# Kernel optimization log

Measured on AMD Instinct MI355X. Metric: run time of the kernel, lower is better.

The kernel has to match this reference:

```python
import jax, jax.numpy as jnp
import numpy as np

B, L, C = 8, 256, 64
NEG = -1e30  # large negative instead of -inf to keep grads NaN-free


def setup_inputs() -> dict:
    key = jax.random.key(0)
    k1, k2 = jax.random.split(key)
    scores = jax.random.normal(k1, (B, L, L, C), dtype=jnp.float32)
    lens = jax.random.randint(k2, (B,), 64, L, dtype=jnp.int32)  # sentence lengths in [64, L-1]
    return {"scores": scores, "lens": lens}


def _inside_max(scores, lens):
    """Max-semiring CKY inside pass. scores: [B,L,L,C]; returns logZ per batch [B]."""
    t = jnp.transpose(jnp.max(scores, axis=-1), (1, 2, 0))  # [L,L,B] best label per span
    s0 = jnp.zeros((L, L, B), scores.dtype)                 # chart s[i,j] = best score of span (i,j)
    i = jnp.arange(L)
    j = jnp.arange(L)

    def step(s, w):
        e = jnp.clip(i + w, 0, L - 1)                       # span end, [L]
        k = jnp.clip(i[:, None] + j[None, :], 0, L - 1)     # split points, [L,L]
        left = s[i[:, None], k]                             # s[i, i+j], [L,L,B]
        right = s[k, e[:, None]]                            # s[i+j, i+w], [L,L,B]
        valid = (j[None, :] >= 1) & (j[None, :] < w) & ((i + w) < L)[:, None]
        comb = jnp.max(jnp.where(valid[..., None], left + right, NEG), axis=1)  # [L,B]
        s_l = t[i, e]                                       # label-max span score, [L,B]
        diag = jnp.where(w == 1, s_l, comb + s_l)
        row_ok = ((i + w) < L)[:, None]
        upd = jnp.where(row_ok, diag, s[i, e])
        s = s.at[i, e].set(upd)
        return s, None

    s, _ = jax.lax.scan(step, s0, jnp.arange(1, L))
    lens_c = jnp.clip(lens, 1, L - 1)
    return s[0, lens_c, jnp.arange(B)]                      # logZ (best tree score) per sentence


def reference(scores, lens):
    return _inside_max(scores, lens)
```

## Files before the change

kernel.cpp:

```cpp
#include <hip/hip_runtime.h>

#define LVAL 256
#define T    32
#define ST   36
#define SLAB (T * ST)
#define NB   8
#define NEG  (-1e30f)

#define LDS_FENCE() asm volatile("s_waitcnt lgkmcnt(0)" ::: "memory")

__device__ __forceinline__ size_t sidx(int b, int i, int e) {
    return ((size_t)b << 16) + (i << 8) + e;
}

template<int CTRL>
__device__ __forceinline__ float dpp_max(float v) {
#if __has_builtin(__builtin_amdgcn_mov_dpp)
    int o = __builtin_amdgcn_mov_dpp(__builtin_bit_cast(int, v), CTRL, 0xF, 0xF, true);
    return fmaxf(v, __builtin_bit_cast(float, o));
#else
    return fmaxf(v, __shfl_xor(v, CTRL == 0xB1 ? 1 : 2));
#endif
}

__global__ __launch_bounds__(256) void phase1(const float* __restrict__ scores,
                                              float* __restrict__ s,
                                              int* __restrict__ bar) {
    if (blockIdx.x == 0 && blockIdx.y == 0) {
        for (int k = threadIdx.x; k < 2048; k += 256) bar[k] = 0;
    }
    const int i = blockIdx.x, b = blockIdx.y;
    const int sub = threadIdx.x & 15, slot = threadIdx.x >> 4;
    const float* row = scores + ((((size_t)b * LVAL + i) * LVAL) << 6);
    #pragma unroll 4
    for (int m0 = 0; m0 < LVAL; m0 += 16) {
        const int e = m0 + slot;
        if (e > i) {
            float4 v = *((const float4*)(row + ((size_t)e << 6)) + sub);
            float mx = fmaxf(fmaxf(v.x, v.y), fmaxf(v.z, v.w));
            #pragma unroll
            for (int d = 1; d < 16; d <<= 1) mx = fmaxf(mx, __shfl_xor(mx, d));
            if (sub == 0) s[sidx(b, i, e)] = mx;
        }
    }
}

template<int LP>
__device__ __forceinline__ void diag_step(int lane, int l,
                                          float (*cur)[ST], float (*curT)[ST],
                                          const float (*tb)[ST]) {
    const int cells = T - l;
    const int P = 1 << LP;
    const int c = lane >> LP, p = lane & (P - 1);
    const bool guard = c < cells;
    const int li = guard ? c : 0;
    const int le = guard ? c + l : 0;
    constexpr int NF = 8 >> LP;
    const float tv = tb[li][le];
    float acc = NEG;
    #pragma unroll
    for (int m = 0; m < NF; ++m) {
        const int k0 = 4 * (p + m * P);
        float4 cu = *(const float4*)&cur[li][k0];
        float4 ct = *(const float4*)&curT[le][k0];
        acc = fmaxf(acc, fmaxf(fmaxf(cu.x + ct.x, cu.y + ct.y),
                               fmaxf(cu.z + ct.z, cu.w + ct.w)));
    }
    acc = dpp_max<0xB1>(acc);
    if (LP >= 2) acc = dpp_max<0x4E>(acc);
    const float v = acc + tv;
    if (guard && p == 0) cur[li][le] = v;
    if (guard && p == 1) curT[le][li] = v;
}

template<int LP>
__device__ __forceinline__ void edge_step(int lane, int l, int D,
                                          const float (*Ae)[ST], const float (*BeT)[ST],
                                          float (*cur)[ST], float (*curT)[ST],
                                          const float (*tb)[ST], const float (*pre)[ST]) {
    const int delta = l - (T - 1);
    const int ad = delta < 0 ? -delta : delta;
    const int cells = T - ad;
    const int P = 1 << LP;
    const int c = lane >> LP, p = lane & (P - 1);
    const bool guard = c < cells;
    const int li = guard ? (delta < 0 ? c + ad : c) : 0;
    const int le = guard ? li + delta : 0;
    constexpr int NF = 8 >> LP;
    const float tv = tb[li][le];
    float acc = pre[li][le];
    #pragma unroll
    for (int m = 0; m < NF; ++m) {
        const int k0 = 4 * (p + m * P);
        float4 a  = *(const float4*)&Ae[li][k0];
        float4 ct = *(const float4*)&curT[le][k0];
        float4 cu = *(const float4*)&cur[li][k0];
        float4 bt = *(const float4*)&BeT[le][k0];
        float s0 = fmaxf(fmaxf(a.x + ct.x, a.y + ct.y), fmaxf(a.z + ct.z, a.w + ct.w));
        float s1 = fmaxf(fmaxf(cu.x + bt.x, cu.y + bt.y), fmaxf(cu.z + bt.z, cu.w + bt.w));
        acc = fmaxf(acc, fmaxf(s0, s1));
    }
    acc = dpp_max<0xB1>(acc);
    if (LP >= 2) acc = dpp_max<0x4E>(acc);
    const float v = (D == 1 && l == 0) ? tv : acc + tv;
    if (guard && p == 0) cur[li][le] = v;
    if (guard && p == 1) curT[le][li] = v;
}

__device__ __forceinline__ void batch_barrier(int* __restrict__ bar, int b,
                                              int tid, int ep) {
    __syncthreads();
    if (tid == 0) {
        int* cnt  = bar + b * 256;
        int* flag = bar + b * 256 + 64;
        __threadfence();
        int prev = __hip_atomic_fetch_add(cnt, 1, __ATOMIC_ACQ_REL,
                                          __HIP_MEMORY_SCOPE_AGENT);
        if (prev == NB - 1) {
            __hip_atomic_store(cnt, 0, __ATOMIC_RELAXED, __HIP_MEMORY_SCOPE_AGENT);
            __hip_atomic_store(flag, ep, __ATOMIC_RELEASE, __HIP_MEMORY_SCOPE_AGENT);
        } else {
            int guard = 0;
            while (__hip_atomic_load(flag, __ATOMIC_RELAXED,
                                     __HIP_MEMORY_SCOPE_AGENT) < ep) {
                __builtin_amdgcn_s_sleep(2);
                if (++guard > (1 << 22)) break;
            }
        }
        __threadfence();
    }
    __syncthreads();
}

__global__ __launch_bounds__(256) void dp_fused(float* __restrict__ s,
                                                const int* __restrict__ lens,
                                                float* __restrict__ out,
                                                int* __restrict__ bar) {
    __shared__ __align__(16) float smem[14 * SLAB];
    float* ATb = smem;
    float (*Ae)[ST]  = (float(*)[ST])(smem + 6 * SLAB);
    float (*tb)[ST]  = (float(*)[ST])(smem + 7 * SLAB);
    float (*BeT)[ST] = (float(*)[ST])(smem + 8 * SLAB);
    float (*cur)[ST] = (float(*)[ST])(smem + 9 * SLAB);
    float* BWb = smem + 10 * SLAB;
    float (*pre)[ST] = (float(*)[ST])BWb;

    const int b  = blockIdx.x & 7;
    const int bi = blockIdx.x >> 3;
    const int tid = threadIdx.x, wid = tid >> 6, lane = tid & 63;
    const int lr = tid >> 5, lc = tid & 31;
    const int grow = lane >> 1, gc = (lane & 1) * 16;
    const int gly = lane >> 3, glx = lane & 7, r0 = 4 * gly, c0 = 4 * glx;
    const int trow = tid >> 3, tc4 = (tid & 7) * 4;
    float (*BW)[ST] = (float(*)[ST])(BWb + wid * SLAB);

    if (wid == 0) {
        float (*curT0)[ST] = (float(*)[ST])(BWb + 1 * SLAB);
        float (*t0)[ST]    = (float(*)[ST])(BWb + 2 * SLAB);
        const float4 negv = make_float4(NEG, NEG, NEG, NEG);
        #pragma unroll
        for (int j = 0; j < 4; ++j) {
            float4 v = *(const float4*)&s[sidx(b, bi * T + grow, bi * T + gc + 4 * j)];
            *(float4*)&t0[grow][gc + 4 * j]    = v;
            *(float4*)&Ae[grow][gc + 4 * j]    = negv;
            *(float4*)&curT0[grow][gc + 4 * j] = negv;
        }
        LDS_FENCE();
        if (lane < T - 1) {
            float v = t0[lane][lane + 1];
            Ae[lane][lane + 1] = v;
            curT0[lane + 1][lane] = v;
        }
        LDS_FENCE();
        #pragma unroll 1
        for (int l = 2; l < T; ++l) {
            if (T - l <= 16) diag_step<2>(lane, l, Ae, curT0, t0);
            else             diag_step<1>(lane, l, Ae, curT0, t0);
            LDS_FENCE();
        }
        #pragma unroll
        for (int j = 0; j < 4; ++j)
            *(float4*)&s[sidx(b, bi * T + grow, bi * T + gc + 4 * j)] =
                *(const float4*)&Ae[grow][gc + 4 * j];
    } else if (bi + 1 < NB) {
        for (int idx = tid - 64; idx < 256; idx += 192) {
            const int row = idx >> 3, c4 = (idx & 7) * 4;
            *(float4*)&tb[row][c4] =
                *(const float4*)&s[sidx(b, bi * T + row, (bi + 1) * T + c4)];
        }
    }

    #pragma unroll 1
    for (int D = 1; D < NB; ++D) {
        batch_barrier(bar, b, tid, D);
        const int be = bi + D;
        if (be < NB) {
            if (D == 1) {
                float4 v = *(const float4*)&s[sidx(b, be * T + trow, be * T + tc4)];
                BeT[tc4 + 0][trow] = (trow < tc4 + 0) ? v.x : NEG;
                BeT[tc4 + 1][trow] = (trow < tc4 + 1) ? v.y : NEG;
                BeT[tc4 + 2][trow] = (trow < tc4 + 2) ? v.z : NEG;
                BeT[tc4 + 3][trow] = (trow < tc4 + 3) ? v.w : NEG;
            }
            const int nw = (D - 1 < 4) ? (D - 1) : 4;
            float ag[4][4];
            #pragma unroll
            for (int i = 0; i < 4; ++i)
                #pragma unroll
                for (int j = 0; j < 4; ++j) ag[i][j] = NEG;
            for (int K = bi + 1 + wid; K < be; K += 4) {
                const float (*AT)[ST] = (const float(*)[ST])(ATb + (K - bi - 1) * SLAB);
                #pragma unroll
                for (int j = 0; j < 4; ++j) {
                    float4 bv = *(const float4*)&s[sidx(b, K * T + grow, be * T + gc + 4 * j)];
                    *(float4*)&BW[grow][gc + 4 * j] = bv;
                }
                LDS_FENCE();
                #pragma unroll 4
                for (int k = 0; k < T; ++k) {
                    float4 a4 = *(const float4*)&AT[k][r0];
                    float4 b4 = *(const float4*)&BW[k][c0];
                    const float aa[4] = {a4.x, a4.y, a4.z, a4.w};
                    const float bb[4] = {b4.x, b4.y, b4.z, b4.w};
                    #pragma unroll
                    for (int i = 0; i < 4; ++i)
                        #pragma unroll
                        for (int j = 0; j < 4; ++j)
                            ag[i][j] = fmaxf(ag[i][j], aa[i] + bb[j]);
                }
                LDS_FENCE();
            }
            if (wid < nw) {
                #pragma unroll
                for (int i = 0; i < 4; ++i)
                    *(float4*)&BW[r0 + i][c0] =
                        make_float4(ag[i][0], ag[i][1], ag[i][2], ag[i][3]);
            }
            __syncthreads();
            #pragma unroll
            for (int r = 0; r < 4; ++r) {
                const int row = lr + 8 * r;
                float v = NEG;
                for (int w2 = 0; w2 < nw; ++w2)
                    v = fmaxf(v, BWb[w2 * SLAB + row * ST + lc]);
                pre[row][lc] = v;
            }
            __syncthreads();
            float (*curT)[ST] = (D == NB - 1) ? (float(*)[ST])(BWb + 1 * SLAB)
                                              : (float(*)[ST])(ATb + (D - 1) * SLAB);
            #pragma unroll
            for (int r = 0; r < 4; ++r) {
                const int row = lr + 8 * r;
                cur[row][lc]  = NEG;
                curT[row][lc] = NEG;
            }
            __syncthreads();
            if (wid == 0) {
                #pragma unroll 1
                for (int l = 0; l < 2 * T - 1; ++l) {
                    const int ad0 = (l < T - 1) ? (T - 1 - l) : (l - (T - 1));
                    if (ad0 >= 16) edge_step<2>(lane, l, D, Ae, BeT, cur, curT, tb, pre);
                    else           edge_step<1>(lane, l, D, Ae, BeT, cur, curT, tb, pre);
                    LDS_FENCE();
                }
            }
            __syncthreads();
            #pragma unroll
            for (int r = 0; r < 4; ++r)
                s[sidx(b, bi * T + lr + 8 * r, be * T + lc)] = cur[lr + 8 * r][lc];
            if (be + 1 < NB) {
                *(float4*)&tb[trow][tc4] =
                    *(const float4*)&s[sidx(b, bi * T + trow, (be + 1) * T + tc4)];
                float4 v = *(const float4*)&s[sidx(b, (be + 1) * T + trow,
                                                   (be + 1) * T + tc4)];
                BeT[tc4 + 0][trow] = (trow < tc4 + 0) ? v.x : NEG;
                BeT[tc4 + 1][trow] = (trow < tc4 + 1) ? v.y : NEG;
                BeT[tc4 + 2][trow] = (trow < tc4 + 2) ? v.z : NEG;
                BeT[tc4 + 3][trow] = (trow < tc4 + 3) ? v.w : NEG;
            }
        }
    }

    if (bi == 0 && tid == 0) {
        int len = lens[b];
        len = len < 1 ? 1 : (len > LVAL - 1 ? LVAL - 1 : len);
        const int K = len >> 5, off = len & 31;
        float r;
        if (K == 0)           r = Ae[0][off];
        else if (K == NB - 1) r = cur[0][off];
        else                  r = ATb[(K - 1) * SLAB + off * ST];
        out[b] = r;
    }
}

extern "C" void kernel_launch(void* const* d_in, const int* in_sizes, int n_in,
                              void* d_out, int out_size, void* d_ws, size_t ws_size,
                              hipStream_t stream) {
    const float* scores = (const float*)d_in[0];
    const int*   lens   = (const int*)d_in[1];
    float*       out    = (float*)d_out;
    float*       s      = (float*)d_ws;
    int*         bar    = (int*)((char*)d_ws + ((size_t)(8) << 16) * sizeof(float));

    phase1<<<dim3(LVAL, 8), 256, 0, stream>>>(scores, s, bar);
    dp_fused<<<64, 256, 0, stream>>>(s, lens, out, bar);
}
```

Measured before the change: 354.6 us.

## Replace threadfences with coherent sc0/sc1 global accesses and relaxed barrier atomics

Removes the __threadfence calls and acquire/release ordering from the inter-block batch barrier. Cross-block chart data is instead read and written with sc0 sc1 cache-coherent global loads and stores, and the counter reset is dropped in favour of a modulo check. It also swaps the explicit LDS waitcnt fences for compiler-only barriers and vectorises the chart store into float4. The aim is to cut fence and cache-flush cost on the serial dependency chain. The risk is a correctness failure if LDS ordering within a wave or global visibility across blocks is no longer guaranteed.

```diff
diff --git a/kernel.cpp b/kernel.cpp
--- a/kernel.cpp
+++ b/kernel.cpp
@@ -7,10 +7,34 @@
 #define NB   8
 #define NEG  (-1e30f)
 
-#define LDS_FENCE() asm volatile("s_waitcnt lgkmcnt(0)" ::: "memory")
+typedef float f32x4 __attribute__((ext_vector_type(4)));
+
+#define SOFT_FENCE() asm volatile("" ::: "memory")
 
 __device__ __forceinline__ size_t sidx(int b, int i, int e) {
     return ((size_t)b << 16) + (i << 8) + e;
+}
+
+__device__ __forceinline__ void st_coh4(float* p, f32x4 v) {
+    asm volatile("global_store_dwordx4 %0, %1, off sc0 sc1"
+                 :: "v"(p), "v"(v) : "memory");
+}
+__device__ __forceinline__ f32x4 ld_coh4(const float* p) {
+    f32x4 v;
+    asm volatile("global_load_dwordx4 %0, %1, off sc0 sc1\n\t"
+                 "s_waitcnt vmcnt(0)"
+                 : "=&v"(v) : "v"(p) : "memory");
+    return v;
+}
+__device__ __forceinline__ void ld_coh4x4(const float* p,
+                                          f32x4& a, f32x4& b, f32x4& c, f32x4& d) {
+    asm volatile("global_load_dwordx4 %0, %4, off sc0 sc1\n\t"
+                 "global_load_dwordx4 %1, %4, off offset:16 sc0 sc1\n\t"
+                 "global_load_dwordx4 %2, %4, off offset:32 sc0 sc1\n\t"
+                 "global_load_dwordx4 %3, %4, off offset:48 sc0 sc1\n\t"
+                 "s_waitcnt vmcnt(0)"
+                 : "=&v"(a), "=&v"(b), "=&v"(c), "=&v"(d)
+                 : "v"(p) : "memory");
 }
 
 template<int CTRL>
@@ -109,16 +133,15 @@
 
 __device__ __forceinline__ void batch_barrier(int* __restrict__ bar, int b,
                                               int tid, int ep) {
+    asm volatile("s_waitcnt vmcnt(0)" ::: "memory");
     __syncthreads();
     if (tid == 0) {
         int* cnt  = bar + b * 256;
         int* flag = bar + b * 256 + 64;
-        __threadfence();
-        int prev = __hip_atomic_fetch_add(cnt, 1, __ATOMIC_ACQ_REL,
+        int prev = __hip_atomic_fetch_add(cnt, 1, __ATOMIC_RELAXED,
                                           __HIP_MEMORY_SCOPE_AGENT);
-        if (prev == NB - 1) {
-            __hip_atomic_store(cnt, 0, __ATOMIC_RELAXED, __HIP_MEMORY_SCOPE_AGENT);
-            __hip_atomic_store(flag, ep, __ATOMIC_RELEASE, __HIP_MEMORY_SCOPE_AGENT);
+        if ((prev & (NB - 1)) == NB - 1) {
+            __hip_atomic_store(flag, ep, __ATOMIC_RELAXED, __HIP_MEMORY_SCOPE_AGENT);
         } else {
             int guard = 0;
             while (__hip_atomic_load(flag, __ATOMIC_RELAXED,
@@ -127,7 +150,6 @@
                 if (++guard > (1 << 22)) break;
             }
         }
-        __threadfence();
     }
     __syncthreads();
 }
@@ -165,23 +187,23 @@
             *(float4*)&Ae[grow][gc + 4 * j]    = negv;
             *(float4*)&curT0[grow][gc + 4 * j] = negv;
         }
-        LDS_FENCE();
+        SOFT_FENCE();
         if (lane < T - 1) {
             float v = t0[lane][lane + 1];
             Ae[lane][lane + 1] = v;
             curT0[lane + 1][lane] = v;
         }
-        LDS_FENCE();
+        SOFT_FENCE();
         #pragma unroll 1
         for (int l = 2; l < T; ++l) {
             if (T - l <= 16) diag_step<2>(lane, l, Ae, curT0, t0);
             else             diag_step<1>(lane, l, Ae, curT0, t0);
-            LDS_FENCE();
+            SOFT_FENCE();
         }
         #pragma unroll
         for (int j = 0; j < 4; ++j)
-            *(float4*)&s[sidx(b, bi * T + grow, bi * T + gc + 4 * j)] =
-                *(const float4*)&Ae[grow][gc + 4 * j];
+            st_coh4(&s[sidx(b, bi * T + grow, bi * T + gc + 4 * j)],
+                    *(const f32x4*)&Ae[grow][gc + 4 * j]);
     } else if (bi + 1 < NB) {
         for (int idx = tid - 64; idx < 256; idx += 192) {
             const int row = idx >> 3, c4 = (idx & 7) * 4;
@@ -196,11 +218,11 @@
         const int be = bi + D;
         if (be < NB) {
             if (D == 1) {
-                float4 v = *(const float4*)&s[sidx(b, be * T + trow, be * T + tc4)];
-                BeT[tc4 + 0][trow] = (trow < tc4 + 0) ? v.x : NEG;
-                BeT[tc4 + 1][trow] = (trow < tc4 + 1) ? v.y : NEG;
-                BeT[tc4 + 2][trow] = (trow < tc4 + 2) ? v.z : NEG;
-                BeT[tc4 + 3][trow] = (trow < tc4 + 3) ? v.w : NEG;
+                f32x4 v = ld_coh4(&s[sidx(b, be * T + trow, be * T + tc4)]);
+                BeT[tc4 + 0][trow] = (trow < tc4 + 0) ? v[0] : NEG;
+                BeT[tc4 + 1][trow] = (trow < tc4 + 1) ? v[1] : NEG;
+                BeT[tc4 + 2][trow] = (trow < tc4 + 2) ? v[2] : NEG;
+                BeT[tc4 + 3][trow] = (trow < tc4 + 3) ? v[3] : NEG;
             }
             const int nw = (D - 1 < 4) ? (D - 1) : 4;
             float ag[4][4];
@@ -210,12 +232,13 @@
                 for (int j = 0; j < 4; ++j) ag[i][j] = NEG;
             for (int K = bi + 1 + wid; K < be; K += 4) {
                 const float (*AT)[ST] = (const float(*)[ST])(ATb + (K - bi - 1) * SLAB);
-                #pragma unroll
-                for (int j = 0; j < 4; ++j) {
-                    float4 bv = *(const float4*)&s[sidx(b, K * T + grow, be * T + gc + 4 * j)];
-                    *(float4*)&BW[grow][gc + 4 * j] = bv;
-                }
-                LDS_FENCE();
+                f32x4 b0, b1, b2, b3;
+                ld_coh4x4(&s[sidx(b, K * T + grow, be * T + gc)], b0, b1, b2, b3);
+                *(f32x4*)&BW[grow][gc + 0]  = b0;
+                *(f32x4*)&BW[grow][gc + 4]  = b1;
+                *(f32x4*)&BW[grow][gc + 8]  = b2;
+                *(f32x4*)&BW[grow][gc + 12] = b3;
+                SOFT_FENCE();
                 #pragma unroll 4
                 for (int k = 0; k < T; ++k) {
                     float4 a4 = *(const float4*)&AT[k][r0];
@@ -228,7 +251,7 @@
                         for (int j = 0; j < 4; ++j)
                             ag[i][j] = fmaxf(ag[i][j], aa[i] + bb[j]);
                 }
-                LDS_FENCE();
+                SOFT_FENCE();
             }
             if (wid < nw) {
                 #pragma unroll
@@ -261,22 +284,23 @@
                     const int ad0 = (l < T - 1) ? (T - 1 - l) : (l - (T - 1));
                     if (ad0 >= 16) edge_step<2>(lane, l, D, Ae, BeT, cur, curT, tb, pre);
                     else           edge_step<1>(lane, l, D, Ae, BeT, cur, curT, tb, pre);
-                    LDS_FENCE();
+                    SOFT_FENCE();
                 }
             }
             __syncthreads();
-            #pragma unroll
-            for (int r = 0; r < 4; ++r)
-                s[sidx(b, bi * T + lr + 8 * r, be * T + lc)] = cur[lr + 8 * r][lc];
+            {
+                f32x4 pv = *(const f32x4*)&cur[trow][tc4];
+                st_coh4(&s[sidx(b, bi * T + trow, be * T + tc4)], pv);
+            }
             if (be + 1 < NB) {
                 *(float4*)&tb[trow][tc4] =
                     *(const float4*)&s[sidx(b, bi * T + trow, (be + 1) * T + tc4)];
-                float4 v = *(const float4*)&s[sidx(b, (be + 1) * T + trow,
-                                                   (be + 1) * T + tc4)];
-                BeT[tc4 + 0][trow] = (trow < tc4 + 0) ? v.x : NEG;
-                BeT[tc4 + 1][trow] = (trow < tc4 + 1) ? v.y : NEG;
-                BeT[tc4 + 2][trow] = (trow < tc4 + 2) ? v.z : NEG;
-                BeT[tc4 + 3][trow] = (trow < tc4 + 3) ? v.w : NEG;
+                f32x4 v = ld_coh4(&s[sidx(b, (be + 1) * T + trow,
+                                          (be + 1) * T + tc4)]);
+                BeT[tc4 + 0][trow] = (trow < tc4 + 0) ? v[0] : NEG;
+                BeT[tc4 + 1][trow] = (trow < tc4 + 1) ? v[1] : NEG;
+                BeT[tc4 + 2][trow] = (trow < tc4 + 2) ? v[2] : NEG;
+                BeT[tc4 + 3][trow] = (trow < tc4 + 3) ? v[3] : NEG;
             }
         }
     }
```

After: 339.0 us. 4.4% less time.
